# Performance work log

Hardware: AMD Instinct MI355X
Metric: run time of the kernel (lower is better)

Reference implementation:

```python
import jax, jax.numpy as jnp
import numpy as np
from jax import lax

INPUT_DIM = 64
HIDDEN = 128
NUM_CLASSES = 3


def _uniform(key, shape, scale):
    return jax.random.uniform(key, shape, jnp.float32, -scale, scale)


def setup_inputs() -> dict:
    key = jax.random.key(0)
    ks = jax.random.split(key, 16)
    s = 1.0 / np.sqrt(HIDDEN)
    inp = {
        "x": jax.random.normal(ks[0], (256, 512, INPUT_DIM), jnp.float32),
        # layer 0 LSTM params (PyTorch gate order: i, f, g, o)
        "W_ih0": _uniform(ks[1], (4 * HIDDEN, INPUT_DIM), s),
        "W_hh0": _uniform(ks[2], (4 * HIDDEN, HIDDEN), s),
        "b_ih0": _uniform(ks[3], (4 * HIDDEN,), s),
        "b_hh0": _uniform(ks[4], (4 * HIDDEN,), s),
        # layer 1 LSTM params
        "W_ih1": _uniform(ks[5], (4 * HIDDEN, HIDDEN), s),
        "W_hh1": _uniform(ks[6], (4 * HIDDEN, HIDDEN), s),
        "b_ih1": _uniform(ks[7], (4 * HIDDEN,), s),
        "b_hh1": _uniform(ks[8], (4 * HIDDEN,), s),
        # MLP head: fc1 (H -> H//2), fc2 (H//2 -> num_classes)
        "W1": _uniform(ks[9], (HIDDEN // 2, HIDDEN), s),
        "b1": _uniform(ks[10], (HIDDEN // 2,), s),
        "W2": _uniform(ks[11], (NUM_CLASSES, HIDDEN // 2), 1.0 / np.sqrt(HIDDEN // 2)),
        "b2": _uniform(ks[12], (NUM_CLASSES,), 1.0 / np.sqrt(HIDDEN // 2)),
    }
    return inp


def _lstm_layer(x, W_ih, W_hh, b_ih, b_hh):
    # x: [B, T, I] -> ys: [B, T, H]
    B = x.shape[0]
    H = W_hh.shape[1]
    b = b_ih + b_hh

    def step(carry, xt):
        h, c = carry
        g = xt @ W_ih.T + h @ W_hh.T + b  # [B, 4H]
        i, f, gg, o = jnp.split(g, 4, axis=-1)
        c = jax.nn.sigmoid(f) * c + jax.nn.sigmoid(i) * jnp.tanh(gg)
        h = jax.nn.sigmoid(o) * jnp.tanh(c)
        return (h, c), h

    h0 = jnp.zeros((B, H), x.dtype)
    (_, _), ys = lax.scan(step, (h0, h0), jnp.swapaxes(x, 0, 1))
    return jnp.swapaxes(ys, 0, 1)


def reference(x, W_ih0, W_hh0, b_ih0, b_hh0, W_ih1, W_hh1, b_ih1, b_hh1, W1, b1, W2, b2):
    # Eval mode: dropout layers are identity.
    h = _lstm_layer(x, W_ih0, W_hh0, b_ih0, b_hh0)   # [B, T, H]
    h = _lstm_layer(h, W_ih1, W_hh1, b_ih1, b_hh1)   # [B, T, H]
    last = h[:, -1, :]                                # [B, H]
    out = jax.nn.relu(last @ W1.T + b1) @ W2.T + b2   # [B, num_classes]
    return out
```

## Files before the change

### kernel.cpp

```cpp
#include <hip/hip_runtime.h>
#include <hip/hip_bf16.h>
#include <stdint.h>

#define BATCH 256
#define SEQ   512
#define INDIM 64
#define H     128
#define RB    4
#define NTILE (BATCH / RB)
#define CH    16
#define NCH   (SEQ / CH)

using short8  = __attribute__((ext_vector_type(8))) short;
using float4v = __attribute__((ext_vector_type(4))) float;

#define LOG2E 1.4426950408889634f

__device__ __forceinline__ unsigned short f2bf(float f) {
    union { float f; uint32_t u; } v; v.f = f;
    uint32_t u = v.u;
    return (unsigned short)((u + 0x7FFFu + ((u >> 16) & 1u)) >> 16);
}

__device__ __forceinline__ float fast_exp2(float x) {
#if __has_builtin(__builtin_amdgcn_exp2f)
    return __builtin_amdgcn_exp2f(x);
#else
    return __expf(x * 0.6931471805599453f);
#endif
}
__device__ __forceinline__ float fast_rcp(float x) {
#if __has_builtin(__builtin_amdgcn_rcpf)
    return __builtin_amdgcn_rcpf(x);
#else
    return 1.f / x;
#endif
}
__device__ __forceinline__ float sigmoid_fast(float x) {
    return fast_rcp(1.f + fast_exp2(-LOG2E * x));
}
__device__ __forceinline__ float tanh_fast(float x) {
    return fmaf(-2.f, fast_rcp(1.f + fast_exp2((2.f * LOG2E) * x)), 1.f);
}

__global__ void conv_x_kernel(const float* __restrict__ x,
                              unsigned short* __restrict__ xb, int n4,
                              int* __restrict__ flags) {
    int i = blockIdx.x * blockDim.x + threadIdx.x;
    if (blockIdx.x == 0 && threadIdx.x < NTILE) flags[threadIdx.x] = 0;
    if (i >= n4) return;
    float4 f = ((const float4*)x)[i];
    ushort4 o;
    o.x = f2bf(f.x); o.y = f2bf(f.y); o.z = f2bf(f.z); o.w = f2bf(f.w);
    ((ushort4*)xb)[i] = o;
}

template<int KIN, bool IS_PROD>
__device__ __forceinline__ void lstm_body(
    const unsigned short* __restrict__ xin,
    const float* __restrict__ Wih,
    const float* __restrict__ Whh,
    const float* __restrict__ b_ih, const float* __restrict__ b_hh,
    unsigned short* __restrict__ outseq,
    const float* __restrict__ W1, const float* __restrict__ b1,
    const float* __restrict__ W2, const float* __restrict__ b2,
    float* __restrict__ out,
    int* flag, int bt)
{
    constexpr int KT  = KIN / 32;
    constexpr int PAD = 132;
    const int lane = threadIdx.x & 63;
    const int quad = lane >> 4;
    const int l16  = lane & 15;
    const int b0   = bt * RB;
    const int cell = (threadIdx.x >> 6) * 16 + l16;
    const int arow = l16 & 12;
    const int xrow = b0 + (l16 >> 2);

    __shared__ short hbuf[2][16][PAD];
    __shared__ float hl[RB][128];
    __shared__ float mid[RB][65];
    for (int i = threadIdx.x; i < 2 * 16 * PAD; i += 512) ((short*)hbuf)[i] = 0;

    short8 whh_f[4][4];
    short8 wih_f[4][KT];
    float  bias[4];
#pragma unroll
    for (int tT = 0; tT < 4; tT++) {
        const int n = tT * 128 + cell;
#pragma unroll
        for (int kt = 0; kt < 4; kt++) {
            const float* p = Whh + (size_t)n * H + kt * 32 + quad * 8;
            float4 f0 = *(const float4*)p;
            float4 f1 = *(const float4*)(p + 4);
            short8 s;
            s[0]=f2bf(f0.x); s[1]=f2bf(f0.y); s[2]=f2bf(f0.z); s[3]=f2bf(f0.w);
            s[4]=f2bf(f1.x); s[5]=f2bf(f1.y); s[6]=f2bf(f1.z); s[7]=f2bf(f1.w);
            whh_f[tT][kt] = s;
        }
#pragma unroll
        for (int kt = 0; kt < KT; kt++) {
            const float* p = Wih + (size_t)n * KIN + kt * 32 + quad * 8;
            float4 f0 = *(const float4*)p;
            float4 f1 = *(const float4*)(p + 4);
            short8 s;
            s[0]=f2bf(f0.x); s[1]=f2bf(f0.y); s[2]=f2bf(f0.z); s[3]=f2bf(f0.w);
            s[4]=f2bf(f1.x); s[5]=f2bf(f1.y); s[6]=f2bf(f1.z); s[7]=f2bf(f1.w);
            wih_f[tT][kt] = s;
        }
        bias[tT] = b_ih[n] + b_hh[n];
    }

    float c0 = 0.f;

    const unsigned short* xp = xin + ((size_t)xrow * SEQ) * KIN + quad * 8;
    unsigned short* op = nullptr;
    if (IS_PROD)
        op = outseq + ((size_t)(b0 + quad) * SEQ) * H + cell;

    short8 xf0[KT], xf1[KT];
    __syncthreads();

    auto step = [&](int t, int cur, short8 (&xuse)[KT], short8 (&xpre)[KT], bool do_pre) {
        if (do_pre) {
            const unsigned short* p = xp + (size_t)(t + 1) * KIN;
#pragma unroll
            for (int kt = 0; kt < KT; kt++) xpre[kt] = *(const short8*)(p + kt * 32);
        }
        short8 ha[4];
#pragma unroll
        for (int kt = 0; kt < 4; kt++)
            ha[kt] = *(const short8*)&hbuf[cur][arow][kt * 32 + quad * 8];

        float4v acc[4];
#pragma unroll
        for (int tT = 0; tT < 4; tT++)
            acc[tT] = (float4v){bias[tT], bias[tT], bias[tT], bias[tT]};
#pragma unroll
        for (int tT = 0; tT < 4; tT++) {
#pragma unroll
            for (int kt = 0; kt < KT; kt++)
                acc[tT] = __builtin_amdgcn_mfma_f32_16x16x32_bf16(xuse[kt], wih_f[tT][kt], acc[tT], 0, 0, 0);
#pragma unroll
            for (int kt = 0; kt < 4; kt++)
                acc[tT] = __builtin_amdgcn_mfma_f32_16x16x32_bf16(ha[kt], whh_f[tT][kt], acc[tT], 0, 0, 0);
        }

        {
            float si = sigmoid_fast(acc[0][0]);
            float sf = sigmoid_fast(acc[1][0]);
            float tg = tanh_fast(acc[2][0]);
            float so = sigmoid_fast(acc[3][0]);
            float cn = fmaf(sf, c0, si * tg);
            c0 = cn;
            float h = so * tanh_fast(cn);
            const unsigned short hb = f2bf(h);
            hbuf[cur ^ 1][quad * 4][cell] = (short)hb;
            if (IS_PROD) {
                *op = hb;
                op += H;
            } else if (t == SEQ - 1) {
                hl[quad][cell] = h;
            }
        }
    };

    for (int ch = 0; ch < NCH; ch++) {
        const int t0 = ch * CH;
        if (!IS_PROD) {
            if (threadIdx.x == 0) {
                while (__hip_atomic_load(flag, __ATOMIC_RELAXED, __HIP_MEMORY_SCOPE_AGENT) <= ch)
                    __builtin_amdgcn_s_sleep(2);
                (void)__hip_atomic_load(flag, __ATOMIC_ACQUIRE, __HIP_MEMORY_SCOPE_AGENT);
            }
            __syncthreads();
            const unsigned short* p = xp + (size_t)t0 * KIN;
#pragma unroll
            for (int kt = 0; kt < KT; kt++) xf0[kt] = *(const short8*)(p + kt * 32);
        } else if (ch == 0) {
            const unsigned short* p = xp;
#pragma unroll
            for (int kt = 0; kt < KT; kt++) xf0[kt] = *(const short8*)(p + kt * 32);
        }
#pragma unroll 1
        for (int i = 0; i < CH; i += 2) {
            const int t = t0 + i;
            step(t, 0, xf0, xf1, true);
            __syncthreads();
            const bool pre1 = IS_PROD ? (t + 2 < SEQ) : (i + 2 < CH);
            step(t + 1, 1, xf1, xf0, pre1);
            __syncthreads();
        }
        if (IS_PROD && threadIdx.x == 0)
            __hip_atomic_fetch_add(flag, 1, __ATOMIC_RELEASE, __HIP_MEMORY_SCOPE_AGENT);
    }

    if (!IS_PROD) {
        if (threadIdx.x < RB * 64) {
            const int row = threadIdx.x >> 6, j = threadIdx.x & 63;
            float s = b1[j];
            const float* wr = W1 + (size_t)j * 128;
#pragma unroll 8
            for (int k = 0; k < 128; k++) s = fmaf(hl[row][k], wr[k], s);
            mid[row][j] = fmaxf(s, 0.f);
        }
        __syncthreads();
        if (threadIdx.x < RB * 3) {
            const int row = threadIdx.x / 3, k = threadIdx.x - row * 3;
            float o = b2[k];
            const float* wr = W2 + (size_t)k * 64;
#pragma unroll 8
            for (int j = 0; j < 64; j++) o = fmaf(mid[row][j], wr[j], o);
            out[(size_t)(b0 + row) * 3 + k] = o;
        }
    }
}

__global__ __launch_bounds__(512, 2)
void lstm_fused_kernel(const unsigned short* __restrict__ xb,
                       const float* __restrict__ Wih0, const float* __restrict__ Whh0,
                       const float* __restrict__ bih0, const float* __restrict__ bhh0,
                       const float* __restrict__ Wih1, const float* __restrict__ Whh1,
                       const float* __restrict__ bih1, const float* __restrict__ bhh1,
                       unsigned short* __restrict__ h0sq,
                       const float* __restrict__ W1, const float* __restrict__ b1,
                       const float* __restrict__ W2, const float* __restrict__ b2,
                       float* __restrict__ out,
                       int* __restrict__ flags)
{
    const int bt = blockIdx.x & (NTILE - 1);
    if (blockIdx.x < NTILE)
        lstm_body<64,  true >(xb,   Wih0, Whh0, bih0, bhh0, h0sq,
                              W1, b1, W2, b2, out, flags + bt, bt);
    else
        lstm_body<128, false>(h0sq, Wih1, Whh1, bih1, bhh1, nullptr,
                              W1, b1, W2, b2, out, flags + bt, bt);
}

extern "C" void kernel_launch(void* const* d_in, const int* in_sizes, int n_in,
                              void* d_out, int out_size, void* d_ws, size_t ws_size,
                              hipStream_t stream) {
    const float* x     = (const float*)d_in[0];
    const float* W_ih0 = (const float*)d_in[1];
    const float* W_hh0 = (const float*)d_in[2];
    const float* b_ih0 = (const float*)d_in[3];
    const float* b_hh0 = (const float*)d_in[4];
    const float* W_ih1 = (const float*)d_in[5];
    const float* W_hh1 = (const float*)d_in[6];
    const float* b_ih1 = (const float*)d_in[7];
    const float* b_hh1 = (const float*)d_in[8];
    const float* W1    = (const float*)d_in[9];
    const float* b1    = (const float*)d_in[10];
    const float* W2    = (const float*)d_in[11];
    const float* b2    = (const float*)d_in[12];
    float* out = (float*)d_out;

    char* ws = (char*)d_ws;
    unsigned short* xb    = (unsigned short*)ws;
    unsigned short* h0sq  = (unsigned short*)(ws + 16777216);
    int*            flags = (int*)(ws + 50331648);

    conv_x_kernel<<<8192, 256, 0, stream>>>(x, xb, (BATCH * SEQ * INDIM) / 4, flags);
    lstm_fused_kernel<<<2 * NTILE, 512, 0, stream>>>(xb, W_ih0, W_hh0, b_ih0, b_hh0,
                                                     W_ih1, W_hh1, b_ih1, b_hh1,
                                                     h0sq, W1, b1, W2, b2, out, flags);
}
```

Before: 529.6 us.

## Offload input-gate GEMMs to helper blocks with ring buffers and flag pipelining

Adds 64 helper blocks that compute the input-projection gates (x·W_ih and h0·W_ih1) per 16-step chunk into double-buffered global rings, so the recurrent blocks only do the W_hh MFMAs per step. Weights are pre-converted to bf16 and biases summed in a separate prep kernel, and per-step syncs use a lighter barrier. The aim is to shorten the serial per-step critical path, at the cost of extra global traffic for fp32 gate rings and more inter-block flag spinning, which needs all 192 blocks co-resident.

```diff
diff --git a/kernel.cpp b/kernel.cpp
--- a/kernel.cpp
+++ b/kernel.cpp
@@ -7,9 +7,23 @@
 #define INDIM 64
 #define H     128
 #define RB    4
-#define NTILE (BATCH / RB)
+#define NTILE 64
 #define CH    16
 #define NCH   (SEQ / CH)
+#define RD    2
+
+#define WS_XB     0u
+#define WS_H0RING 16777216u
+#define WS_G0RING 18874368u
+#define WS_G1RING 35651584u
+#define WS_WB     52428800u
+#define WS_BSUM   52887552u
+#define WS_FLAGS  52891648u
+#define WB_IH0 0
+#define WB_HH0 32768
+#define WB_IH1 98304
+#define WB_HH1 163840
+#define WB_TOT 229376
 
 using short8  = __attribute__((ext_vector_type(8))) short;
 using float4v = __attribute__((ext_vector_type(4))) float;
@@ -21,7 +35,6 @@
     uint32_t u = v.u;
     return (unsigned short)((u + 0x7FFFu + ((u >> 16) & 1u)) >> 16);
 }
-
 __device__ __forceinline__ float fast_exp2(float x) {
 #if __has_builtin(__builtin_amdgcn_exp2f)
     return __builtin_amdgcn_exp2f(x);
@@ -42,162 +55,186 @@
 __device__ __forceinline__ float tanh_fast(float x) {
     return fmaf(-2.f, fast_rcp(1.f + fast_exp2((2.f * LOG2E) * x)), 1.f);
 }
-
-__global__ void conv_x_kernel(const float* __restrict__ x,
-                              unsigned short* __restrict__ xb, int n4,
-                              int* __restrict__ flags) {
+__device__ __forceinline__ void light_barrier() {
+    asm volatile("s_waitcnt lgkmcnt(0)\n\ts_barrier" ::: "memory");
+}
+__device__ __forceinline__ void spin_ge(const int* f, int target) {
+    while (__hip_atomic_load(f, __ATOMIC_RELAXED, __HIP_MEMORY_SCOPE_AGENT) < target)
+        __builtin_amdgcn_s_sleep(2);
+    (void)__hip_atomic_load(f, __ATOMIC_ACQUIRE, __HIP_MEMORY_SCOPE_AGENT);
+}
+__device__ __forceinline__ void bump(int* f) {
+    __hip_atomic_fetch_add(f, 1, __ATOMIC_RELEASE, __HIP_MEMORY_SCOPE_AGENT);
+}
+
+__global__ void conv_x_kernel(const float* __restrict__ x, unsigned short* __restrict__ xb) {
     int i = blockIdx.x * blockDim.x + threadIdx.x;
-    if (blockIdx.x == 0 && threadIdx.x < NTILE) flags[threadIdx.x] = 0;
-    if (i >= n4) return;
     float4 f = ((const float4*)x)[i];
     ushort4 o;
     o.x = f2bf(f.x); o.y = f2bf(f.y); o.z = f2bf(f.z); o.w = f2bf(f.w);
     ((ushort4*)xb)[i] = o;
 }
 
-template<int KIN, bool IS_PROD>
-__device__ __forceinline__ void lstm_body(
-    const unsigned short* __restrict__ xin,
-    const float* __restrict__ Wih,
-    const float* __restrict__ Whh,
-    const float* __restrict__ b_ih, const float* __restrict__ b_hh,
-    unsigned short* __restrict__ outseq,
+__global__ void prep_w_kernel(const float* __restrict__ Wih0, const float* __restrict__ Whh0,
+                              const float* __restrict__ Wih1, const float* __restrict__ Whh1,
+                              const float* __restrict__ bih0, const float* __restrict__ bhh0,
+                              const float* __restrict__ bih1, const float* __restrict__ bhh1,
+                              unsigned short* __restrict__ wb, float* __restrict__ bsum,
+                              int* __restrict__ flags) {
+    int gid = blockIdx.x * blockDim.x + threadIdx.x;
+    float v;
+    if      (gid < WB_HH0) v = Wih0[gid];
+    else if (gid < WB_IH1) v = Whh0[gid - WB_HH0];
+    else if (gid < WB_HH1) v = Wih1[gid - WB_IH1];
+    else                   v = Whh1[gid - WB_HH1];
+    wb[gid] = f2bf(v);
+    if (gid < 512)       bsum[gid] = bih0[gid] + bhh0[gid];
+    else if (gid < 1024) bsum[gid] = bih1[gid - 512] + bhh1[gid - 512];
+    if (gid < 256) flags[gid] = 0;
+}
+
+template<bool L0>
+__device__ __forceinline__ void gates_gemm(
+    const unsigned short* __restrict__ abase,
+    const unsigned short* __restrict__ wih,
+    const float* __restrict__ bsum,
+    float* __restrict__ gslot,
+    int b0, int t0, int w, int lane)
+{
+    constexpr int K  = L0 ? INDIM : H;
+    constexpr int KT = K / 32;
+    const int quad = lane >> 4, l16 = lane & 15;
+
+    short8 af[4][KT];
+#pragma unroll
+    for (int mt = 0; mt < 4; mt++) {
+        const int m = mt * 16 + l16;
+        const unsigned short* ap = L0
+            ? abase + ((size_t)(b0 + (m & 3)) * SEQ + (t0 + (m >> 2))) * INDIM + quad * 8
+            : abase + (size_t)m * H + quad * 8;
+#pragma unroll
+        for (int kt = 0; kt < KT; kt++) af[mt][kt] = *(const short8*)(ap + kt * 32);
+    }
+#pragma unroll
+    for (int j = 0; j < 4; j++) {
+        const int n = (w * 4 + j) * 16 + l16;
+        short8 bf[KT];
+#pragma unroll
+        for (int kt = 0; kt < KT; kt++)
+            bf[kt] = *(const short8*)(wih + (size_t)n * K + kt * 32 + quad * 8);
+        const float bs = bsum[n];
+        const int cellc = n & 127, tT = n >> 7;
+#pragma unroll
+        for (int mt = 0; mt < 4; mt++) {
+            float4v acc = (float4v){bs, bs, bs, bs};
+#pragma unroll
+            for (int kt = 0; kt < KT; kt++)
+                acc = __builtin_amdgcn_mfma_f32_16x16x32_bf16(af[mt][kt], bf[kt], acc, 0, 0, 0);
+#pragma unroll
+            for (int reg = 0; reg < 4; reg++) {
+                const int m_out = mt * 16 + quad * 4 + reg;
+                const int io = m_out >> 2, ro = m_out & 3;
+                const int tidr = (cellc >> 4) * 64 + ro * 16 + (cellc & 15);
+                gslot[((size_t)io * 512 + tidr) * 4 + tT] = acc[reg];
+            }
+        }
+    }
+}
+
+template<bool IS_PROD>
+__device__ __forceinline__ void lstm_rec(
+    const unsigned short* __restrict__ wb_hh,
+    const float* __restrict__ gring,
+    unsigned short* __restrict__ h0ring,
     const float* __restrict__ W1, const float* __restrict__ b1,
     const float* __restrict__ W2, const float* __restrict__ b2,
     float* __restrict__ out,
-    int* flag, int bt)
+    int* g0rdy, int* g1rdy, int* prodprog, int* consprog, int bt)
 {
-    constexpr int KT  = KIN / 32;
-    constexpr int PAD = 132;
-    const int lane = threadIdx.x & 63;
-    const int quad = lane >> 4;
-    const int l16  = lane & 15;
+    const int tid  = threadIdx.x;
+    const int lane = tid & 63, w = tid >> 6, quad = lane >> 4, l16 = lane & 15;
     const int b0   = bt * RB;
-    const int cell = (threadIdx.x >> 6) * 16 + l16;
+    const int cell = w * 16 + l16;
     const int arow = l16 & 12;
-    const int xrow = b0 + (l16 >> 2);
-
-    __shared__ short hbuf[2][16][PAD];
+
+    __shared__ short hbuf[2][16][132];
     __shared__ float hl[RB][128];
     __shared__ float mid[RB][65];
-    for (int i = threadIdx.x; i < 2 * 16 * PAD; i += 512) ((short*)hbuf)[i] = 0;
+    for (int i = tid; i < 2 * 16 * 132; i += 512) ((short*)hbuf)[i] = 0;
 
     short8 whh_f[4][4];
-    short8 wih_f[4][KT];
-    float  bias[4];
-#pragma unroll
-    for (int tT = 0; tT < 4; tT++) {
-        const int n = tT * 128 + cell;
+#pragma unroll
+    for (int tT = 0; tT < 4; tT++)
+#pragma unroll
+        for (int kt = 0; kt < 4; kt++)
+            whh_f[tT][kt] = *(const short8*)(wb_hh + (size_t)(tT * 128 + cell) * H + kt * 32 + quad * 8);
+
+    const float4* gbase = (const float4*)gring + (size_t)bt * (RD * CH * 512);
+    unsigned short* hbase = IS_PROD ? h0ring + (size_t)bt * (RD * CH * RB * H) : nullptr;
+
+    float  c0 = 0.f;
+    float4 giA, giB;
+    __syncthreads();
+
+    auto rstep = [&](int i, int CUR, float4& gi,
+                     const float4* gs, unsigned short* hs, bool doPre, bool lastStep)
+        __attribute__((always_inline)) {
+        short8 ha[4];
+#pragma unroll
+        for (int kt = 0; kt < 4; kt++)
+            ha[kt] = *(const short8*)&hbuf[CUR][arow][kt * 32 + quad * 8];
+        float4v a0 = (float4v){gi.x, 0.f, 0.f, 0.f};
+        float4v a1 = (float4v){gi.y, 0.f, 0.f, 0.f};
+        float4v a2 = (float4v){gi.z, 0.f, 0.f, 0.f};
+        float4v a3 = (float4v){gi.w, 0.f, 0.f, 0.f};
 #pragma unroll
         for (int kt = 0; kt < 4; kt++) {
-            const float* p = Whh + (size_t)n * H + kt * 32 + quad * 8;
-            float4 f0 = *(const float4*)p;
-            float4 f1 = *(const float4*)(p + 4);
-            short8 s;
-            s[0]=f2bf(f0.x); s[1]=f2bf(f0.y); s[2]=f2bf(f0.z); s[3]=f2bf(f0.w);
-            s[4]=f2bf(f1.x); s[5]=f2bf(f1.y); s[6]=f2bf(f1.z); s[7]=f2bf(f1.w);
-            whh_f[tT][kt] = s;
-        }
-#pragma unroll
-        for (int kt = 0; kt < KT; kt++) {
-            const float* p = Wih + (size_t)n * KIN + kt * 32 + quad * 8;
-            float4 f0 = *(const float4*)p;
-            float4 f1 = *(const float4*)(p + 4);
-            short8 s;
-            s[0]=f2bf(f0.x); s[1]=f2bf(f0.y); s[2]=f2bf(f0.z); s[3]=f2bf(f0.w);
-            s[4]=f2bf(f1.x); s[5]=f2bf(f1.y); s[6]=f2bf(f1.z); s[7]=f2bf(f1.w);
-            wih_f[tT][kt] = s;
-        }
-        bias[tT] = b_ih[n] + b_hh[n];
-    }
-
-    float c0 = 0.f;
-
-    const unsigned short* xp = xin + ((size_t)xrow * SEQ) * KIN + quad * 8;
-    unsigned short* op = nullptr;
-    if (IS_PROD)
-        op = outseq + ((size_t)(b0 + quad) * SEQ) * H + cell;
-
-    short8 xf0[KT], xf1[KT];
-    __syncthreads();
-
-    auto step = [&](int t, int cur, short8 (&xuse)[KT], short8 (&xpre)[KT], bool do_pre) {
-        if (do_pre) {
-            const unsigned short* p = xp + (size_t)(t + 1) * KIN;
-#pragma unroll
-            for (int kt = 0; kt < KT; kt++) xpre[kt] = *(const short8*)(p + kt * 32);
-        }
-        short8 ha[4];
-#pragma unroll
-        for (int kt = 0; kt < 4; kt++)
-            ha[kt] = *(const short8*)&hbuf[cur][arow][kt * 32 + quad * 8];
-
-        float4v acc[4];
-#pragma unroll
-        for (int tT = 0; tT < 4; tT++)
-            acc[tT] = (float4v){bias[tT], bias[tT], bias[tT], bias[tT]};
-#pragma unroll
-        for (int tT = 0; tT < 4; tT++) {
-#pragma unroll
-            for (int kt = 0; kt < KT; kt++)
-                acc[tT] = __builtin_amdgcn_mfma_f32_16x16x32_bf16(xuse[kt], wih_f[tT][kt], acc[tT], 0, 0, 0);
-#pragma unroll
-            for (int kt = 0; kt < 4; kt++)
-                acc[tT] = __builtin_amdgcn_mfma_f32_16x16x32_bf16(ha[kt], whh_f[tT][kt], acc[tT], 0, 0, 0);
-        }
-
-        {
-            float si = sigmoid_fast(acc[0][0]);
-            float sf = sigmoid_fast(acc[1][0]);
-            float tg = tanh_fast(acc[2][0]);
-            float so = sigmoid_fast(acc[3][0]);
-            float cn = fmaf(sf, c0, si * tg);
-            c0 = cn;
-            float h = so * tanh_fast(cn);
-            const unsigned short hb = f2bf(h);
-            hbuf[cur ^ 1][quad * 4][cell] = (short)hb;
-            if (IS_PROD) {
-                *op = hb;
-                op += H;
-            } else if (t == SEQ - 1) {
-                hl[quad][cell] = h;
-            }
-        }
+            a0 = __builtin_amdgcn_mfma_f32_16x16x32_bf16(ha[kt], whh_f[0][kt], a0, 0, 0, 0);
+            a1 = __builtin_amdgcn_mfma_f32_16x16x32_bf16(ha[kt], whh_f[1][kt], a1, 0, 0, 0);
+            a2 = __builtin_amdgcn_mfma_f32_16x16x32_bf16(ha[kt], whh_f[2][kt], a2, 0, 0, 0);
+            a3 = __builtin_amdgcn_mfma_f32_16x16x32_bf16(ha[kt], whh_f[3][kt], a3, 0, 0, 0);
+        }
+        if (doPre) gi = gs[(size_t)(i + 2) * 512 + tid];
+        float si = sigmoid_fast(a0[0]);
+        float sf = sigmoid_fast(a1[0]);
+        float tg = tanh_fast(a2[0]);
+        float so = sigmoid_fast(a3[0]);
+        float cn = fmaf(sf, c0, si * tg);
+        c0 = cn;
+        float h = so * tanh_fast(cn);
+        const unsigned short hb = f2bf(h);
+        hbuf[CUR ^ 1][quad * 4][cell] = (short)hb;
+        if (IS_PROD) {
+            hs[(size_t)(i * 4 + quad) * H + cell] = hb;
+        } else if (lastStep) {
+            hl[quad][cell] = h;
+        }
+        light_barrier();
     };
 
     for (int ch = 0; ch < NCH; ch++) {
-        const int t0 = ch * CH;
-        if (!IS_PROD) {
-            if (threadIdx.x == 0) {
-                while (__hip_atomic_load(flag, __ATOMIC_RELAXED, __HIP_MEMORY_SCOPE_AGENT) <= ch)
-                    __builtin_amdgcn_s_sleep(2);
-                (void)__hip_atomic_load(flag, __ATOMIC_ACQUIRE, __HIP_MEMORY_SCOPE_AGENT);
-            }
-            __syncthreads();
-            const unsigned short* p = xp + (size_t)t0 * KIN;
-#pragma unroll
-            for (int kt = 0; kt < KT; kt++) xf0[kt] = *(const short8*)(p + kt * 32);
-        } else if (ch == 0) {
-            const unsigned short* p = xp;
-#pragma unroll
-            for (int kt = 0; kt < KT; kt++) xf0[kt] = *(const short8*)(p + kt * 32);
-        }
+        if (tid == 0) {
+            spin_ge(IS_PROD ? &g0rdy[bt] : &g1rdy[bt], ch + 1);
+            if (IS_PROD && ch >= 2) spin_ge(&g1rdy[bt], ch - 1);
+        }
+        __syncthreads();
+        const float4*   gs = gbase + (size_t)(ch & 1) * (CH * 512);
+        unsigned short* hs = IS_PROD ? hbase + (size_t)(ch & 1) * (CH * RB * H) : nullptr;
+        giA = gs[tid];
+        giB = gs[512 + tid];
+        const bool lastCh = (ch == NCH - 1);
 #pragma unroll 1
         for (int i = 0; i < CH; i += 2) {
-            const int t = t0 + i;
-            step(t, 0, xf0, xf1, true);
-            __syncthreads();
-            const bool pre1 = IS_PROD ? (t + 2 < SEQ) : (i + 2 < CH);
-            step(t + 1, 1, xf1, xf0, pre1);
-            __syncthreads();
-        }
-        if (IS_PROD && threadIdx.x == 0)
-            __hip_atomic_fetch_add(flag, 1, __ATOMIC_RELEASE, __HIP_MEMORY_SCOPE_AGENT);
+            rstep(i,     0, giA, gs, hs, i + 2 < CH, false);
+            rstep(i + 1, 1, giB, gs, hs, i + 3 < CH, lastCh && (i + 1 == CH - 1));
+        }
+        __syncthreads();
+        if (tid == 0) bump(IS_PROD ? &prodprog[bt] : &consprog[bt]);
     }
 
     if (!IS_PROD) {
-        if (threadIdx.x < RB * 64) {
-            const int row = threadIdx.x >> 6, j = threadIdx.x & 63;
+        if (tid < RB * 64) {
+            const int row = tid >> 6, j = tid & 63;
             float s = b1[j];
             const float* wr = W1 + (size_t)j * 128;
 #pragma unroll 8
@@ -205,8 +242,8 @@
             mid[row][j] = fmaxf(s, 0.f);
         }
         __syncthreads();
-        if (threadIdx.x < RB * 3) {
-            const int row = threadIdx.x / 3, k = threadIdx.x - row * 3;
+        if (tid < RB * 3) {
+            const int row = tid / 3, k = tid - row * 3;
             float o = b2[k];
             const float* wr = W2 + (size_t)k * 64;
 #pragma unroll 8
@@ -216,25 +253,69 @@
     }
 }
 
+__device__ __forceinline__ void helper_body(
+    const unsigned short* __restrict__ xb, const unsigned short* __restrict__ h0ring,
+    const unsigned short* __restrict__ wb, const float* __restrict__ bsum,
+    float* __restrict__ g0ring, float* __restrict__ g1ring,
+    int* g0rdy, int* g1rdy, int* prodprog, int* consprog, int bt)
+{
+    const int tid = threadIdx.x, w = tid >> 6, lane = tid & 63;
+    const int b0 = bt * RB;
+    float* g0base = g0ring + (size_t)bt * (RD * CH * 512 * 4);
+    float* g1base = g1ring + (size_t)bt * (RD * CH * 512 * 4);
+    const unsigned short* h0base = h0ring + (size_t)bt * (RD * CH * RB * H);
+
+    for (int ch = 0; ch < NCH; ch++) {
+        if (ch >= 2) { if (tid == 0) spin_ge(&prodprog[bt], ch - 1); __syncthreads(); }
+        gates_gemm<true>(xb, wb + WB_IH0, bsum,
+                         g0base + (size_t)(ch & 1) * (CH * 512 * 4), b0, ch * CH, w, lane);
+        __syncthreads();
+        if (tid == 0) bump(&g0rdy[bt]);
+        if (ch >= 1) {
+            const int c1 = ch - 1;
+            if (tid == 0) { spin_ge(&prodprog[bt], c1 + 1); if (c1 >= 2) spin_ge(&consprog[bt], c1 - 1); }
+            __syncthreads();
+            gates_gemm<false>(h0base + (size_t)(c1 & 1) * (CH * RB * H), wb + WB_IH1, bsum + 512,
+                              g1base + (size_t)(c1 & 1) * (CH * 512 * 4), b0, 0, w, lane);
+            __syncthreads();
+            if (tid == 0) bump(&g1rdy[bt]);
+        }
+    }
+    {
+        const int c1 = NCH - 1;
+        if (tid == 0) { spin_ge(&prodprog[bt], c1 + 1); spin_ge(&consprog[bt], c1 - 1); }
+        __syncthreads();
+        gates_gemm<false>(h0base + (size_t)(c1 & 1) * (CH * RB * H), wb + WB_IH1, bsum + 512,
+                          g1base + (size_t)(c1 & 1) * (CH * 512 * 4), b0, 0, w, lane);
+        __syncthreads();
+        if (tid == 0) bump(&g1rdy[bt]);
+    }
+}
+
 __global__ __launch_bounds__(512, 2)
 void lstm_fused_kernel(const unsigned short* __restrict__ xb,
-                       const float* __restrict__ Wih0, const float* __restrict__ Whh0,
-                       const float* __restrict__ bih0, const float* __restrict__ bhh0,
-                       const float* __restrict__ Wih1, const float* __restrict__ Whh1,
-                       const float* __restrict__ bih1, const float* __restrict__ bhh1,
-                       unsigned short* __restrict__ h0sq,
+                       const unsigned short* __restrict__ wb,
+                       const float* __restrict__ bsum,
+                       float* __restrict__ g0ring, float* __restrict__ g1ring,
+                       unsigned short* __restrict__ h0ring,
                        const float* __restrict__ W1, const float* __restrict__ b1,
                        const float* __restrict__ W2, const float* __restrict__ b2,
-                       float* __restrict__ out,
-                       int* __restrict__ flags)
+                       float* __restrict__ out, int* __restrict__ flags)
 {
-    const int bt = blockIdx.x & (NTILE - 1);
-    if (blockIdx.x < NTILE)
-        lstm_body<64,  true >(xb,   Wih0, Whh0, bih0, bhh0, h0sq,
-                              W1, b1, W2, b2, out, flags + bt, bt);
-    else
-        lstm_body<128, false>(h0sq, Wih1, Whh1, bih1, bhh1, nullptr,
-                              W1, b1, W2, b2, out, flags + bt, bt);
+    int* g0rdy    = flags;
+    int* g1rdy    = flags + 64;
+    int* prodprog = flags + 128;
+    int* consprog = flags + 192;
+    if (blockIdx.x < 64) {
+        lstm_rec<true >(wb + WB_HH0, g0ring, h0ring, W1, b1, W2, b2, out,
+                        g0rdy, g1rdy, prodprog, consprog, blockIdx.x);
+    } else if (blockIdx.x < 128) {
+        lstm_rec<false>(wb + WB_HH1, g1ring, nullptr, W1, b1, W2, b2, out,
+                        g0rdy, g1rdy, prodprog, consprog, blockIdx.x - 64);
+    } else {
+        helper_body(xb, h0ring, wb, bsum, g0ring, g1ring,
+                    g0rdy, g1rdy, prodprog, consprog, blockIdx.x - 128);
+    }
 }
 
 extern "C" void kernel_launch(void* const* d_in, const int* in_sizes, int n_in,
@@ -256,12 +337,17 @@
     float* out = (float*)d_out;
 
     char* ws = (char*)d_ws;
-    unsigned short* xb    = (unsigned short*)ws;
-    unsigned short* h0sq  = (unsigned short*)(ws + 16777216);
-    int*            flags = (int*)(ws + 50331648);
-
-    conv_x_kernel<<<8192, 256, 0, stream>>>(x, xb, (BATCH * SEQ * INDIM) / 4, flags);
-    lstm_fused_kernel<<<2 * NTILE, 512, 0, stream>>>(xb, W_ih0, W_hh0, b_ih0, b_hh0,
-                                                     W_ih1, W_hh1, b_ih1, b_hh1,
-                                                     h0sq, W1, b1, W2, b2, out, flags);
-}
+    unsigned short* xb   = (unsigned short*)(ws + WS_XB);
+    unsigned short* h0r  = (unsigned short*)(ws + WS_H0RING);
+    float*          g0r  = (float*)(ws + WS_G0RING);
+    float*          g1r  = (float*)(ws + WS_G1RING);
+    unsigned short* wb   = (unsigned short*)(ws + WS_WB);
+    float*          bsum = (float*)(ws + WS_BSUM);
+    int*            flags= (int*)(ws + WS_FLAGS);
+
+    conv_x_kernel<<<8192, 256, 0, stream>>>(x, xb);
+    prep_w_kernel<<<896, 256, 0, stream>>>(W_ih0, W_hh0, W_ih1, W_hh1,
+                                           b_ih0, b_hh0, b_ih1, b_hh1, wb, bsum, flags);
+    lstm_fused_kernel<<<192, 512, 0, stream>>>(xb, wb, bsum, g0r, g1r, h0r,
+                                               W1, b1, W2, b2, out, flags);
+}
```

Measured after the change: 1.170 ms. +120.9%, slower.
